# Optimization experiments

Measured on AMD Instinct MI355X. Metric: run time of the kernel, lower is better.

The kernel has to match this reference:

```python
import jax, jax.numpy as jnp
import numpy as np

EMB = 256
IN_CH = 256
CTX_D = 128


def setup_inputs() -> dict:
    key = jax.random.key(0)
    ks = jax.random.split(key, 12)
    b, c, h, w = 16, IN_CH, 48, 48
    seq = 2048
    s = 0.02
    return {
        "x": jax.random.normal(ks[0], (b, c, h, w), jnp.float32),
        "context": jax.random.normal(ks[1], (b, seq, CTX_D), jnp.float32),
        "pad_mask": jax.random.bernoulli(ks[2], 0.1, (b, h * w, seq)),
        "W_in": jax.random.normal(ks[3], (EMB, IN_CH), jnp.float32) * s,   # 1x1 conv weight
        "b_in": jnp.zeros((EMB,), jnp.float32),
        "Wq": jax.random.normal(ks[4], (EMB, EMB), jnp.float32) * s,
        "bq": jnp.zeros((EMB,), jnp.float32),
        "Wk": jax.random.normal(ks[5], (EMB, CTX_D), jnp.float32) * s,
        "bk": jnp.zeros((EMB,), jnp.float32),
        "Wv": jax.random.normal(ks[6], (EMB, CTX_D), jnp.float32) * s,
        "bv": jnp.zeros((EMB,), jnp.float32),
        "W_out": jax.random.normal(ks[7], (IN_CH, EMB), jnp.float32) * s,  # 1x1 conv weight
        "b_out": jnp.zeros((IN_CH,), jnp.float32),
    }


def reference(x, context, pad_mask, W_in, b_in, Wq, bq, Wk, bk, Wv, bv, W_out, b_out):
    b, c, h, w = x.shape
    scale = EMB ** (-0.5)
    # proj_in: 1x1 conv == channel matmul; then b c h w -> b (h w) c
    xt = jnp.einsum('bchw,ec->behw', x, W_in) + b_in[None, :, None, None]
    xt = xt.reshape(b, EMB, h * w).transpose(0, 2, 1)          # [b, hw, emb]
    Q = xt @ Wq.T + bq                                          # [b, hw, emb]
    K = context @ Wk.T + bk                                     # [b, seq, emb]
    V = context @ Wv.T + bv                                     # [b, seq, emb]
    att = jnp.einsum('bid,bjd->bij', Q, K) * scale              # [b, hw, seq]
    att = jnp.where(pad_mask, jnp.float32(-1e9), att)
    att = jax.nn.softmax(att, axis=-1)
    out = jnp.einsum('bij,bjd->bid', att, V)                    # [b, hw, emb]
    out = out.transpose(0, 2, 1).reshape(b, EMB, h, w)
    out = jnp.einsum('behw,ce->bchw', out, W_out) + b_out[None, :, None, None]
    return out, att
```

## Files before the change

### kernel.cpp

```cpp
#include <hip/hip_runtime.h>

typedef unsigned short u16;
typedef unsigned int   u32;
typedef __attribute__((ext_vector_type(8))) __bf16 bf16x8;
typedef __attribute__((ext_vector_type(4))) float  f32x4;

#define BB   16
#define CH   256
#define HW   2304
#define SEQ  2048
#define EMB  256
#define CTXD 128
#define OUT0 9437184

#define MFMA(a,b,c) __builtin_amdgcn_mfma_f32_16x16x32_bf16(a,b,c,0,0,0)

__device__ __forceinline__ u16 f2bf(float f){
  u32 u = __builtin_bit_cast(u32, f);
  u += 0x7fffu + ((u >> 16) & 1u);
  return (u16)(u >> 16);
}
__device__ __forceinline__ float bf2f(u32 us){ return __builtin_bit_cast(float, us << 16); }

__device__ __forceinline__ bf16x8 ld16(const u16* p){
  uint4 q = *reinterpret_cast<const uint4*>(p);
  return __builtin_bit_cast(bf16x8, q);
}
__device__ __forceinline__ bf16x8 ld16c(const char* p){
  uint4 q = *reinterpret_cast<const uint4*>(p);
  return __builtin_bit_cast(bf16x8, q);
}
__device__ __forceinline__ bf16x8 mk8(float a0,float a1,float a2,float a3,
                                      float a4,float a5,float a6,float a7){
  uint4 q;
  q.x = (u32)f2bf(a0) | ((u32)f2bf(a1) << 16);
  q.y = (u32)f2bf(a2) | ((u32)f2bf(a3) << 16);
  q.z = (u32)f2bf(a4) | ((u32)f2bf(a5) << 16);
  q.w = (u32)f2bf(a6) | ((u32)f2bf(a7) << 16);
  return __builtin_bit_cast(bf16x8, q);
}
__device__ __forceinline__ void gload16(const u16* g, u16* l){
  __builtin_amdgcn_global_load_lds(
      (const __attribute__((address_space(1))) unsigned int*)(const void*)g,
      (__attribute__((address_space(3))) unsigned int*)(void*)l, 16, 0, 0);
}

__global__ __launch_bounds__(256) void k_prep(
    const float* __restrict__ Wq, const float* __restrict__ W_in,
    const float* __restrict__ b_in, const float* __restrict__ bq,
    const float* __restrict__ Wk, const float* __restrict__ Wv,
    const float* __restrict__ Wout,
    u16* __restrict__ WqinBf, u16* __restrict__ WkBf, u16* __restrict__ WvBf,
    u16* __restrict__ WoutBf, float* __restrict__ bq_eff)
{
  int blk = blockIdx.x, t = threadIdx.x;
  const float SC = 0.0625f;
  if (blk < 256) {
    int e = blk, c = t;
    float s = 0.f;
    #pragma unroll 8
    for (int f = 0; f < 256; f++) s += Wq[e*256+f] * W_in[f*256+c];
    WqinBf[e*256+c] = f2bf(s * SC);
    __shared__ float rb[4];
    float pb = Wq[e*256+t] * b_in[t];
    pb += __shfl_xor(pb, 1);  pb += __shfl_xor(pb, 2);
    pb += __shfl_xor(pb, 4);  pb += __shfl_xor(pb, 8);
    pb += __shfl_xor(pb, 16); pb += __shfl_xor(pb, 32);
    if ((t & 63) == 0) rb[t >> 6] = pb;
    __syncthreads();
    if (t == 0) bq_eff[e] = (rb[0]+rb[1]+rb[2]+rb[3] + bq[e]) * SC;
  } else {
    u32 flat = (u32)(blk - 256) * 256 + t;
    for (u32 idx = flat; idx < 131072u; idx += 16384u) {
      if (idx < 32768u)       WkBf[idx]          = f2bf(Wk[idx]);
      else if (idx < 65536u)  WvBf[idx - 32768u] = f2bf(Wv[idx - 32768u]);
      else                    WoutBf[idx - 65536u] = f2bf(Wout[idx - 65536u]);
    }
  }
}

__global__ __launch_bounds__(256) void k_qproj(
    const float* __restrict__ x, const u16* __restrict__ WqinBf,
    const float* __restrict__ bq_eff, u16* __restrict__ Qbf)
{
  int b = blockIdx.y, ibase = blockIdx.x * 64;
  int t = threadIdx.x, wv = t >> 6, lane = t & 63, g4 = lane >> 4, r16 = lane & 15;
  int e0 = wv * 64;
  f32x4 acc[4][4] = {};
  #pragma unroll 2
  for (int kk = 0; kk < 8; kk++) {
    bf16x8 a[4];
    #pragma unroll
    for (int m = 0; m < 4; m++)
      a[m] = ld16(WqinBf + (size_t)(e0 + m*16 + r16) * 256 + kk*32 + g4*8);
    bf16x8 bb[4];
    #pragma unroll
    for (int n = 0; n < 4; n++) {
      const float* xp = x + ((size_t)b*CH + kk*32 + g4*8) * HW + ibase + n*16 + r16;
      bb[n] = mk8(xp[0], xp[HW], xp[2*HW], xp[3*HW], xp[4*HW], xp[5*HW], xp[6*HW], xp[7*HW]);
    }
    #pragma unroll
    for (int m = 0; m < 4; m++)
      #pragma unroll
      for (int n = 0; n < 4; n++)
        acc[m][n] = MFMA(a[m], bb[n], acc[m][n]);
  }
  #pragma unroll
  for (int m = 0; m < 4; m++) {
    int e = e0 + m*16 + g4*4;
    float b0 = bq_eff[e], b1 = bq_eff[e+1], b2 = bq_eff[e+2], b3 = bq_eff[e+3];
    #pragma unroll
    for (int n = 0; n < 4; n++) {
      int i = ibase + n*16 + r16;
      u32 lo = (u32)f2bf(acc[m][n][0] + b0) | ((u32)f2bf(acc[m][n][1] + b1) << 16);
      u32 hi = (u32)f2bf(acc[m][n][2] + b2) | ((u32)f2bf(acc[m][n][3] + b3) << 16);
      *(uint2*)(Qbf + ((size_t)b*HW + i) * EMB + e) = make_uint2(lo, hi);
    }
  }
}

__global__ __launch_bounds__(512) void k_kvproj(
    const float* __restrict__ ctx, const u16* __restrict__ WkBf, const u16* __restrict__ WvBf,
    const float* __restrict__ bk, const float* __restrict__ bv,
    u16* __restrict__ Kbf, u16* __restrict__ Vtb)
{
  int b = blockIdx.y, sbase = blockIdx.x * 64;
  int t = threadIdx.x, wv = t >> 6, lane = t & 63, g4 = lane >> 4, r16 = lane & 15;
  bool isV = wv >= 4;
  int e0 = (wv & 3) * 64;
  const u16* Wsel = isV ? WvBf : WkBf;
  f32x4 acc[4][4] = {};
  #pragma unroll
  for (int kk = 0; kk < 4; kk++) {
    bf16x8 a[4];
    #pragma unroll
    for (int m = 0; m < 4; m++)
      a[m] = ld16(Wsel + (size_t)(e0 + m*16 + r16) * 128 + kk*32 + g4*8);
    bf16x8 bb[4];
    #pragma unroll
    for (int n = 0; n < 4; n++) {
      const float* cp = ctx + ((size_t)b*SEQ + sbase + n*16 + r16) * CTXD + kk*32 + g4*8;
      float4 lo = *(const float4*)cp;
      float4 hi = *(const float4*)(cp + 4);
      bb[n] = mk8(lo.x, lo.y, lo.z, lo.w, hi.x, hi.y, hi.z, hi.w);
    }
    #pragma unroll
    for (int m = 0; m < 4; m++)
      #pragma unroll
      for (int n = 0; n < 4; n++)
        acc[m][n] = MFMA(a[m], bb[n], acc[m][n]);
  }
  if (!isV) {
    #pragma unroll
    for (int m = 0; m < 4; m++) {
      int e = e0 + m*16 + g4*4;
      float b0 = bk[e], b1 = bk[e+1], b2 = bk[e+2], b3 = bk[e+3];
      #pragma unroll
      for (int n = 0; n < 4; n++) {
        int s = sbase + n*16 + r16;
        u32 lo = (u32)f2bf(acc[m][n][0] + b0) | ((u32)f2bf(acc[m][n][1] + b1) << 16);
        u32 hi = (u32)f2bf(acc[m][n][2] + b2) | ((u32)f2bf(acc[m][n][3] + b3) << 16);
        *(uint2*)(Kbf + ((size_t)b*SEQ + s) * EMB + e) = make_uint2(lo, hi);
      }
    }
  } else {
    #pragma unroll
    for (int m = 0; m < 4; m++) {
      #pragma unroll
      for (int r = 0; r < 4; r++) {
        int e = e0 + m*16 + g4*4 + r;
        float bvv = bv[e];
        #pragma unroll
        for (int n = 0; n < 4; n++) {
          int s = sbase + n*16 + r16;
          Vtb[((size_t)b*EMB + e) * SEQ + s] = f2bf(acc[m][n][r] + bvv);
        }
      }
    }
  }
}

__global__ __launch_bounds__(512, 4) void k_qk(
    const u16* __restrict__ Qbf, const u16* __restrict__ Kbf,
    const int* __restrict__ mask, float* __restrict__ dout,
    float* __restrict__ gpart)
{
  __shared__ u16 lsA[128*64];
  __shared__ u16 lsB[128*64];
  __shared__ float red[4][128];

  int bid = blockIdx.x;
  int work = (bid & 7) * 576 + (bid >> 3);
  int b = work / 288, rem = work % 288;
  int mt = rem / 16, jt = rem % 16;
  int mbase = mt * 128, jbase = jt * 128;
  size_t bH = (size_t)b * HW, bS = (size_t)b * SEQ;

  int t = threadIdx.x, lane = t & 63, wv = t >> 6, g4 = lane >> 4, r16 = lane & 15;
  int wr = wv >> 2, wc = wv & 3;

  int mreg[4][2][4];
  {
    const int* mp = mask + (bH + mbase + wr*64 + g4*4) * SEQ + jbase + wc*32 + r16;
    #pragma unroll
    for (int m = 0; m < 4; m++)
      #pragma unroll
      for (int n = 0; n < 2; n++)
        #pragma unroll
        for (int r = 0; r < 4; r++)
          mreg[m][n][r] = mp[(size_t)(m*16 + r) * SEQ + n*16];
  }

  int i0 = t, i1 = t + 512;
  int r0 = i0 >> 3, c0 = (i0 & 7) ^ (r0 & 7);
  int r1 = i1 >> 3, c1 = (i1 & 7) ^ (r1 & 7);
  const u16* qs0 = Qbf + (bH + mbase + r0) * 256 + c0*8;
  const u16* qs1 = Qbf + (bH + mbase + r1) * 256 + c1*8;
  const u16* ks0 = Kbf + (bS + jbase + r0) * 256 + c0*8;
  const u16* ks1 = Kbf + (bS + jbase + r1) * 256 + c1*8;
  u16 *dA0 = lsA + i0*8, *dA1 = lsA + i1*8, *dB0 = lsB + i0*8, *dB1 = lsB + i1*8;

  const char* lA = (const char*)lsA;
  const char* lB = (const char*)lsB;

  f32x4 acc[4][2] = {};
  #pragma unroll 1
  for (int ks = 0; ks < 4; ks++) {
    gload16(qs0 + ks*64, dA0);
    gload16(qs1 + ks*64, dA1);
    gload16(ks0 + ks*64, dB0);
    gload16(ks1 + ks*64, dB1);
    __syncthreads();
    #pragma unroll
    for (int kk = 0; kk < 2; kk++) {
      bf16x8 af[4], bf[2];
      #pragma unroll
      for (int m = 0; m < 4; m++) {
        int row = wr*64 + m*16 + r16;
        af[m] = ld16c(lA + row*128 + (((kk<<2)|g4) ^ (row&7))*16);
      }
      #pragma unroll
      for (int n = 0; n < 2; n++) {
        int row = wc*32 + n*16 + r16;
        bf[n] = ld16c(lB + row*128 + (((kk<<2)|g4) ^ (row&7))*16);
      }
      #pragma unroll
      for (int m = 0; m < 4; m++)
        #pragma unroll
        for (int n = 0; n < 2; n++)
          acc[m][n] = MFMA(af[m], bf[n], acc[m][n]);
    }
    __syncthreads();
  }

  u16* Ebase = (u16*)(dout + OUT0);
  float part[4][4] = {};
  #pragma unroll
  for (int m = 0; m < 4; m++)
    #pragma unroll
    for (int n = 0; n < 2; n++)
      #pragma unroll
      for (int r = 0; r < 4; r++) {
        float e = mreg[m][n][r] ? 0.f : __expf(acc[m][n][r]);
        part[m][r] += e;
        int i = wr*64 + m*16 + g4*4 + r;
        int j = jbase + wc*32 + n*16 + r16;
        Ebase[(bH + mbase + i) * 4096 + 2048 + j] = f2bf(e);
      }
  #pragma unroll
  for (int m = 0; m < 4; m++)
    #pragma unroll
    for (int r = 0; r < 4; r++) {
      float v = part[m][r];
      v += __shfl_xor(v, 1); v += __shfl_xor(v, 2);
      v += __shfl_xor(v, 4); v += __shfl_xor(v, 8);
      if (r16 == 0) red[wc][wr*64 + m*16 + g4*4 + r] = v;
    }
  __syncthreads();
  if (t < 128) {
    float tot = red[0][t] + red[1][t] + red[2][t] + red[3][t];
    gpart[(bH + mbase + t) * 16 + jt] = tot;
  }
}

__global__ __launch_bounds__(256, 4) void k_pv(
    const u16* __restrict__ Vtb, const float* __restrict__ gpart,
    float* __restrict__ dout, u16* __restrict__ Obf)
{
  __shared__ u16 lsE[32*64];
  __shared__ u16 lsV[256*64];
  __shared__ float invl[32];

  int bid = blockIdx.x;
  int work = (bid & 7) * 144 + (bid >> 3);
  int b = work / 72, mt = work % 72;
  int mbase = mt * 32;
  size_t bH = (size_t)b * HW;

  int t = threadIdx.x, lane = t & 63, wv = t >> 6, g4 = lane >> 4, r16 = lane & 15;

  if (t < 32) {
    const float4* pp = (const float4*)(gpart + (bH + mbase + t) * 16);
    float4 p0 = pp[0], p1 = pp[1], p2 = pp[2], p3 = pp[3];
    float s = p0.x+p0.y+p0.z+p0.w + p1.x+p1.y+p1.z+p1.w
            + p2.x+p2.y+p2.z+p2.w + p3.x+p3.y+p3.z+p3.w;
    invl[t] = 1.f / s;
  }

  const u16* Ebase = (const u16*)(dout + OUT0);
  float* attb = dout + OUT0;
  int rE = t >> 3, cE = (t & 7) ^ (rE & 7);
  const u16* esrc = Ebase + (bH + mbase + rE) * 4096 + 2048 + cE*8;
  u16* dE = lsE + t*8;
  int rV[8], cV[8];
  #pragma unroll
  for (int i = 0; i < 8; i++) {
    int idx = i*256 + t;
    rV[i] = idx >> 3;
    cV[i] = (idx & 7) ^ (rV[i] & 7);
  }
  const char* lE = (const char*)lsE;
  const char* lV = (const char*)lsV;
  int srow = t >> 3;
  u32 sxor = (u32)((t & 7) ^ (srow & 7)) * 16;
  float* arow = attb + (bH + mbase + srow) * 2048 + (t & 7) * 8;

  f32x4 acc[2][4] = {};
  #pragma unroll 1
  for (int c = 0; c < 32; c++) {
    int kb = c * 64;
    gload16(esrc + kb, dE);
    #pragma unroll
    for (int i = 0; i < 8; i++)
      gload16(Vtb + ((size_t)b*EMB + rV[i]) * SEQ + kb + cV[i]*8, lsV + (i*256 + t)*8);
    __syncthreads();
    #pragma unroll
    for (int kk = 0; kk < 2; kk++) {
      bf16x8 aE[2], bV[4];
      #pragma unroll
      for (int m = 0; m < 2; m++) {
        int row = m*16 + r16;
        aE[m] = ld16c(lE + row*128 + (((kk<<2)|g4) ^ (row&7))*16);
      }
      #pragma unroll
      for (int n = 0; n < 4; n++) {
        int row = wv*64 + n*16 + r16;
        bV[n] = ld16c(lV + row*128 + (((kk<<2)|g4) ^ (row&7))*16);
      }
      #pragma unroll
      for (int m = 0; m < 2; m++)
        #pragma unroll
        for (int n = 0; n < 4; n++)
          acc[m][n] = MFMA(aE[m], bV[n], acc[m][n]);
    }
    {
      float iv = invl[srow];
      const u16* ep = (const u16*)(lE + srow*128 + sxor);
      float4 o0, o1;
      o0.x = bf2f(ep[0]) * iv; o0.y = bf2f(ep[1]) * iv;
      o0.z = bf2f(ep[2]) * iv; o0.w = bf2f(ep[3]) * iv;
      o1.x = bf2f(ep[4]) * iv; o1.y = bf2f(ep[5]) * iv;
      o1.z = bf2f(ep[6]) * iv; o1.w = bf2f(ep[7]) * iv;
      *(float4*)(arow + kb) = o0;
      *(float4*)(arow + kb + 4) = o1;
    }
    __syncthreads();
  }

  #pragma unroll
  for (int m = 0; m < 2; m++)
    #pragma unroll
    for (int n = 0; n < 4; n++)
      #pragma unroll
      for (int r = 0; r < 4; r++) {
        int i = m*16 + g4*4 + r;
        int e = wv*64 + n*16 + r16;
        Obf[(bH + mbase + i) * 256 + e] = f2bf(acc[m][n][r] * invl[i]);
      }
}

__global__ __launch_bounds__(256) void k_outproj(
    const u16* __restrict__ Obf, const u16* __restrict__ WoutBf,
    const float* __restrict__ bout, float* __restrict__ out)
{
  int b = blockIdx.y, ibase = blockIdx.x * 64;
  int t = threadIdx.x, wv = t >> 6, lane = t & 63, g4 = lane >> 4, r16 = lane & 15;
  int c0 = wv * 64;
  f32x4 acc[4][4] = {};
  #pragma unroll 2
  for (int kk = 0; kk < 8; kk++) {
    bf16x8 a[4];
    #pragma unroll
    for (int m = 0; m < 4; m++)
      a[m] = ld16(WoutBf + (size_t)(c0 + m*16 + r16) * 256 + kk*32 + g4*8);
    bf16x8 bb[4];
    #pragma unroll
    for (int n = 0; n < 4; n++)
      bb[n] = ld16(Obf + ((size_t)b*HW + ibase + n*16 + r16) * EMB + kk*32 + g4*8);
    #pragma unroll
    for (int m = 0; m < 4; m++)
      #pragma unroll
      for (int n = 0; n < 4; n++)
        acc[m][n] = MFMA(a[m], bb[n], acc[m][n]);
  }
  #pragma unroll
  for (int m = 0; m < 4; m++) {
    #pragma unroll
    for (int r = 0; r < 4; r++) {
      int c = c0 + m*16 + g4*4 + r;
      float bo = bout[c];
      #pragma unroll
      for (int n = 0; n < 4; n++) {
        int i = ibase + n*16 + r16;
        out[((size_t)b*CH + c) * HW + i] = acc[m][n][r] + bo;
      }
    }
  }
}

extern "C" void kernel_launch(void* const* d_in, const int* in_sizes, int n_in,
                              void* d_out, int out_size, void* d_ws, size_t ws_size,
                              hipStream_t stream)
{
  const float* x    = (const float*)d_in[0];
  const float* ctx  = (const float*)d_in[1];
  const int*   mask = (const int*)  d_in[2];
  const float* W_in = (const float*)d_in[3];
  const float* b_in = (const float*)d_in[4];
  const float* Wq   = (const float*)d_in[5];
  const float* bq   = (const float*)d_in[6];
  const float* Wk   = (const float*)d_in[7];
  const float* bk   = (const float*)d_in[8];
  const float* Wv   = (const float*)d_in[9];
  const float* bv   = (const float*)d_in[10];
  const float* Wout = (const float*)d_in[11];
  const float* bout = (const float*)d_in[12];
  float* out = (float*)d_out;

  char* ws = (char*)d_ws;
  size_t off = 0;
  auto alloc = [&](size_t bytes) -> void* {
    void* p = ws + off;
    off += (bytes + 255) & ~(size_t)255;
    return p;
  };
  u16*   WqinBf = (u16*)  alloc(256*256*2);
  u16*   WkBf   = (u16*)  alloc(256*128*2);
  u16*   WvBf   = (u16*)  alloc(256*128*2);
  u16*   WoutBf = (u16*)  alloc(256*256*2);
  float* bq_eff = (float*)alloc(256*4);
  float* gpart  = (float*)alloc((size_t)BB*HW*16*4);
  u16*   Qbf    = (u16*)  alloc((size_t)BB*HW*EMB*2);
  u16*   Kbf    = (u16*)  alloc((size_t)BB*SEQ*EMB*2);
  u16*   Vtb    = (u16*)  alloc((size_t)BB*EMB*SEQ*2);
  if (off > ws_size) return;

  k_prep<<<dim3(320), dim3(256), 0, stream>>>(Wq, W_in, b_in, bq, Wk, Wv, Wout,
                                              WqinBf, WkBf, WvBf, WoutBf, bq_eff);
  k_qproj<<<dim3(36, 16), dim3(256), 0, stream>>>(x, WqinBf, bq_eff, Qbf);
  k_kvproj<<<dim3(32, 16), dim3(512), 0, stream>>>(ctx, WkBf, WvBf, bk, bv, Kbf, Vtb);
  k_qk<<<dim3(4608), dim3(512), 0, stream>>>(Qbf, Kbf, mask, out, gpart);
  k_pv<<<dim3(1152), dim3(256), 0, stream>>>(Vtb, gpart, out, Qbf );
  k_outproj<<<dim3(36, 16), dim3(256), 0, stream>>>(Qbf , WoutBf, bout, out);
}
```

Baseline: 430.7 us.

## Double-buffer LDS tiles in QK and PV kernels and defer mask loads

```diff
diff --git a/kernel.cpp b/kernel.cpp
--- a/kernel.cpp
+++ b/kernel.cpp
@@ -185,8 +185,8 @@
     const int* __restrict__ mask, float* __restrict__ dout,
     float* __restrict__ gpart)
 {
-  __shared__ u16 lsA[128*64];
-  __shared__ u16 lsB[128*64];
+  __shared__ u16 lsA[2][128*64];
+  __shared__ u16 lsB[2][128*64];
   __shared__ float red[4][128];
 
   int bid = blockIdx.x;
@@ -198,18 +198,6 @@
 
   int t = threadIdx.x, lane = t & 63, wv = t >> 6, g4 = lane >> 4, r16 = lane & 15;
   int wr = wv >> 2, wc = wv & 3;
-
-  int mreg[4][2][4];
-  {
-    const int* mp = mask + (bH + mbase + wr*64 + g4*4) * SEQ + jbase + wc*32 + r16;
-    #pragma unroll
-    for (int m = 0; m < 4; m++)
-      #pragma unroll
-      for (int n = 0; n < 2; n++)
-        #pragma unroll
-        for (int r = 0; r < 4; r++)
-          mreg[m][n][r] = mp[(size_t)(m*16 + r) * SEQ + n*16];
-  }
 
   int i0 = t, i1 = t + 512;
   int r0 = i0 >> 3, c0 = (i0 & 7) ^ (r0 & 7);
@@ -218,19 +206,38 @@
   const u16* qs1 = Qbf + (bH + mbase + r1) * 256 + c1*8;
   const u16* ks0 = Kbf + (bS + jbase + r0) * 256 + c0*8;
   const u16* ks1 = Kbf + (bS + jbase + r1) * 256 + c1*8;
-  u16 *dA0 = lsA + i0*8, *dA1 = lsA + i1*8, *dB0 = lsB + i0*8, *dB1 = lsB + i1*8;
-
-  const char* lA = (const char*)lsA;
-  const char* lB = (const char*)lsB;
+
+  const int* mp = mask + (bH + mbase + wr*64 + g4*4) * SEQ + jbase + wc*32 + r16;
+  int mreg[4][2][4];
 
   f32x4 acc[4][2] = {};
-  #pragma unroll 1
+
+  gload16(qs0, lsA[0] + i0*8);
+  gload16(qs1, lsA[0] + i1*8);
+  gload16(ks0, lsB[0] + i0*8);
+  gload16(ks1, lsB[0] + i1*8);
+  __syncthreads();
+
+  int cur = 0;
+  #pragma unroll
   for (int ks = 0; ks < 4; ks++) {
-    gload16(qs0 + ks*64, dA0);
-    gload16(qs1 + ks*64, dA1);
-    gload16(ks0 + ks*64, dB0);
-    gload16(ks1 + ks*64, dB1);
-    __syncthreads();
+    if (ks < 3) {
+      int nb = cur ^ 1;
+      gload16(qs0 + (ks+1)*64, lsA[nb] + i0*8);
+      gload16(qs1 + (ks+1)*64, lsA[nb] + i1*8);
+      gload16(ks0 + (ks+1)*64, lsB[nb] + i0*8);
+      gload16(ks1 + (ks+1)*64, lsB[nb] + i1*8);
+    } else {
+      #pragma unroll
+      for (int m = 0; m < 4; m++)
+        #pragma unroll
+        for (int n = 0; n < 2; n++)
+          #pragma unroll
+          for (int r = 0; r < 4; r++)
+            mreg[m][n][r] = mp[(size_t)(m*16 + r) * SEQ + n*16];
+    }
+    const char* lA = (const char*)lsA[cur];
+    const char* lB = (const char*)lsB[cur];
     #pragma unroll
     for (int kk = 0; kk < 2; kk++) {
       bf16x8 af[4], bf[2];
@@ -250,7 +257,8 @@
         for (int n = 0; n < 2; n++)
           acc[m][n] = MFMA(af[m], bf[n], acc[m][n]);
     }
-    __syncthreads();
+    if (ks < 3) __syncthreads();
+    cur ^= 1;
   }
 
   u16* Ebase = (u16*)(dout + OUT0);
@@ -283,12 +291,12 @@
   }
 }
 
-__global__ __launch_bounds__(256, 4) void k_pv(
+__global__ __launch_bounds__(256, 2) void k_pv(
     const u16* __restrict__ Vtb, const float* __restrict__ gpart,
     float* __restrict__ dout, u16* __restrict__ Obf)
 {
-  __shared__ u16 lsE[32*64];
-  __shared__ u16 lsV[256*64];
+  __shared__ u16 lsE[2][32*64];
+  __shared__ u16 lsV[2][256*64];
   __shared__ float invl[32];
 
   int bid = blockIdx.x;
@@ -311,7 +319,6 @@
   float* attb = dout + OUT0;
   int rE = t >> 3, cE = (t & 7) ^ (rE & 7);
   const u16* esrc = Ebase + (bH + mbase + rE) * 4096 + 2048 + cE*8;
-  u16* dE = lsE + t*8;
   int rV[8], cV[8];
   #pragma unroll
   for (int i = 0; i < 8; i++) {
@@ -319,21 +326,31 @@
     rV[i] = idx >> 3;
     cV[i] = (idx & 7) ^ (rV[i] & 7);
   }
-  const char* lE = (const char*)lsE;
-  const char* lV = (const char*)lsV;
   int srow = t >> 3;
   u32 sxor = (u32)((t & 7) ^ (srow & 7)) * 16;
   float* arow = attb + (bH + mbase + srow) * 2048 + (t & 7) * 8;
 
+  gload16(esrc, lsE[0] + t*8);
+  #pragma unroll
+  for (int i = 0; i < 8; i++)
+    gload16(Vtb + ((size_t)b*EMB + rV[i]) * SEQ + cV[i]*8, lsV[0] + (i*256 + t)*8);
+  __syncthreads();
+
   f32x4 acc[2][4] = {};
+  int cur = 0;
   #pragma unroll 1
   for (int c = 0; c < 32; c++) {
     int kb = c * 64;
-    gload16(esrc + kb, dE);
-    #pragma unroll
-    for (int i = 0; i < 8; i++)
-      gload16(Vtb + ((size_t)b*EMB + rV[i]) * SEQ + kb + cV[i]*8, lsV + (i*256 + t)*8);
-    __syncthreads();
+    if (c < 31) {
+      int nb = cur ^ 1;
+      gload16(esrc + kb + 64, lsE[nb] + t*8);
+      #pragma unroll
+      for (int i = 0; i < 8; i++)
+        gload16(Vtb + ((size_t)b*EMB + rV[i]) * SEQ + kb + 64 + cV[i]*8,
+                lsV[nb] + (i*256 + t)*8);
+    }
+    const char* lE = (const char*)lsE[cur];
+    const char* lV = (const char*)lsV[cur];
     #pragma unroll
     for (int kk = 0; kk < 2; kk++) {
       bf16x8 aE[2], bV[4];
@@ -364,7 +381,8 @@
       *(float4*)(arow + kb) = o0;
       *(float4*)(arow + kb + 4) = o1;
     }
-    __syncthreads();
+    if (c < 31) __syncthreads();
+    cur ^= 1;
   }
 
   #pragma unroll
```

New measurement: 457.6 us. 1.06x slower.

## Double-buffer E tiles in k_pv, read V directly from global, widen row tile

Applied to the files above, without the earlier changes.

```diff
diff --git a/kernel.cpp b/kernel.cpp
--- a/kernel.cpp
+++ b/kernel.cpp
@@ -283,75 +283,62 @@
   }
 }
 
-__global__ __launch_bounds__(256, 4) void k_pv(
+__global__ __launch_bounds__(512, 6) void k_pv(
     const u16* __restrict__ Vtb, const float* __restrict__ gpart,
     float* __restrict__ dout, u16* __restrict__ Obf)
 {
-  __shared__ u16 lsE[32*64];
-  __shared__ u16 lsV[256*64];
-  __shared__ float invl[32];
+  __shared__ u16 lsE[2][64*64];
+  __shared__ float invl[64];
 
   int bid = blockIdx.x;
-  int work = (bid & 7) * 144 + (bid >> 3);
-  int b = work / 72, mt = work % 72;
-  int mbase = mt * 32;
+  int work = (bid & 7) * 72 + (bid >> 3);
+  int b = work / 36, mt = work % 36;
+  int mbase = mt * 64;
   size_t bH = (size_t)b * HW;
 
   int t = threadIdx.x, lane = t & 63, wv = t >> 6, g4 = lane >> 4, r16 = lane & 15;
-
-  if (t < 32) {
+  int wm = wv >> 2, we = wv & 3;
+
+  if (t < 64) {
     const float4* pp = (const float4*)(gpart + (bH + mbase + t) * 16);
     float4 p0 = pp[0], p1 = pp[1], p2 = pp[2], p3 = pp[3];
-    float s = p0.x+p0.y+p0.z+p0.w + p1.x+p1.y+p1.z+p1.w
-            + p2.x+p2.y+p2.z+p2.w + p3.x+p3.y+p3.z+p3.w;
-    invl[t] = 1.f / s;
+    invl[t] = 1.f / (p0.x+p0.y+p0.z+p0.w + p1.x+p1.y+p1.z+p1.w
+                   + p2.x+p2.y+p2.z+p2.w + p3.x+p3.y+p3.z+p3.w);
   }
 
   const u16* Ebase = (const u16*)(dout + OUT0);
   float* attb = dout + OUT0;
   int rE = t >> 3, cE = (t & 7) ^ (rE & 7);
   const u16* esrc = Ebase + (bH + mbase + rE) * 4096 + 2048 + cE*8;
-  u16* dE = lsE + t*8;
-  int rV[8], cV[8];
-  #pragma unroll
-  for (int i = 0; i < 8; i++) {
-    int idx = i*256 + t;
-    rV[i] = idx >> 3;
-    cV[i] = (idx & 7) ^ (rV[i] & 7);
-  }
-  const char* lE = (const char*)lsE;
-  const char* lV = (const char*)lsV;
+  const u16* Vb = Vtb + (size_t)b * EMB * SEQ;
   int srow = t >> 3;
   u32 sxor = (u32)((t & 7) ^ (srow & 7)) * 16;
   float* arow = attb + (bH + mbase + srow) * 2048 + (t & 7) * 8;
 
+  gload16(esrc, lsE[0] + t*8);
+  __syncthreads();
+
   f32x4 acc[2][4] = {};
+  int cur = 0;
   #pragma unroll 1
   for (int c = 0; c < 32; c++) {
     int kb = c * 64;
-    gload16(esrc + kb, dE);
-    #pragma unroll
-    for (int i = 0; i < 8; i++)
-      gload16(Vtb + ((size_t)b*EMB + rV[i]) * SEQ + kb + cV[i]*8, lsV + (i*256 + t)*8);
-    __syncthreads();
+    if (c < 31) gload16(esrc + kb + 64, lsE[cur ^ 1] + t*8);
+    const char* lE = (const char*)lsE[cur];
     #pragma unroll
     for (int kk = 0; kk < 2; kk++) {
-      bf16x8 aE[2], bV[4];
+      bf16x8 aE[2];
       #pragma unroll
       for (int m = 0; m < 2; m++) {
-        int row = m*16 + r16;
+        int row = wm*32 + m*16 + r16;
         aE[m] = ld16c(lE + row*128 + (((kk<<2)|g4) ^ (row&7))*16);
       }
       #pragma unroll
       for (int n = 0; n < 4; n++) {
-        int row = wv*64 + n*16 + r16;
-        bV[n] = ld16c(lV + row*128 + (((kk<<2)|g4) ^ (row&7))*16);
-      }
-      #pragma unroll
-      for (int m = 0; m < 2; m++)
-        #pragma unroll
-        for (int n = 0; n < 4; n++)
-          acc[m][n] = MFMA(aE[m], bV[n], acc[m][n]);
+        bf16x8 bV = ld16(Vb + (size_t)(we*64 + n*16 + r16) * SEQ + kb + kk*32 + g4*8);
+        acc[0][n] = MFMA(aE[0], bV, acc[0][n]);
+        acc[1][n] = MFMA(aE[1], bV, acc[1][n]);
+      }
     }
     {
       float iv = invl[srow];
@@ -365,6 +352,7 @@
       *(float4*)(arow + kb + 4) = o1;
     }
     __syncthreads();
+    cur ^= 1;
   }
 
   #pragma unroll
@@ -373,8 +361,8 @@
     for (int n = 0; n < 4; n++)
       #pragma unroll
       for (int r = 0; r < 4; r++) {
-        int i = m*16 + g4*4 + r;
-        int e = wv*64 + n*16 + r16;
+        int i = wm*32 + m*16 + g4*4 + r;
+        int e = we*64 + n*16 + r16;
         Obf[(bH + mbase + i) * 256 + e] = f2bf(acc[m][n][r] * invl[i]);
       }
 }
@@ -460,6 +448,6 @@
   k_qproj<<<dim3(36, 16), dim3(256), 0, stream>>>(x, WqinBf, bq_eff, Qbf);
   k_kvproj<<<dim3(32, 16), dim3(512), 0, stream>>>(ctx, WkBf, WvBf, bk, bv, Kbf, Vtb);
   k_qk<<<dim3(4608), dim3(512), 0, stream>>>(Qbf, Kbf, mask, out, gpart);
-  k_pv<<<dim3(1152), dim3(256), 0, stream>>>(Vtb, gpart, out, Qbf );
+  k_pv<<<dim3(576), dim3(512), 0, stream>>>(Vtb, gpart, out, Qbf );
   k_outproj<<<dim3(36, 16), dim3(256), 0, stream>>>(Qbf , WoutBf, bout, out);
 }
```

New measurement: 502.2 us. 16.6% more time.
